# Optimization experiments

Measured on AMD Instinct MI355X. Metric: run time of the kernel, lower is better.

## Reference

```python
import jax, jax.numpy as jnp
import numpy as np

D_MODEL = 512
NUM_HEADS = 8
HEAD_DIM = D_MODEL // NUM_HEADS


def setup_inputs() -> dict:
    key = jax.random.key(0)
    k1, k2, k3, k4, k5 = jax.random.split(key, 5)
    B, S = 4, 2048
    hidden_states = jax.random.normal(k1, (B, S, D_MODEL), dtype=jnp.float32)
    attention_mask = jnp.ones((B, S), dtype=jnp.int32)
    scale = 1.0 / np.sqrt(D_MODEL)
    Wq = jax.random.normal(k2, (D_MODEL, D_MODEL), dtype=jnp.float32) * scale
    Wk = jax.random.normal(k3, (D_MODEL, D_MODEL), dtype=jnp.float32) * scale
    Wv = jax.random.normal(k4, (D_MODEL, D_MODEL), dtype=jnp.float32) * scale
    Wo = jax.random.normal(k5, (D_MODEL, D_MODEL), dtype=jnp.float32) * scale
    return {
        "hidden_states": hidden_states,
        "attention_mask": attention_mask,
        "Wq": Wq, "Wk": Wk, "Wv": Wv, "Wo": Wo,
        "window_size": 256,
    }


def reference(hidden_states, attention_mask, Wq, Wk, Wv, Wo, window_size):
    B, S, _ = hidden_states.shape
    H, Dh = NUM_HEADS, HEAD_DIM
    # torch Linear: y = x @ W.T  (weights are [out, in])
    q = (hidden_states @ Wq.T).reshape(B, S, H, Dh).transpose(0, 2, 1, 3)
    k = (hidden_states @ Wk.T).reshape(B, S, H, Dh).transpose(0, 2, 1, 3)
    v = (hidden_states @ Wv.T).reshape(B, S, H, Dh).transpose(0, 2, 1, 3)
    scores = jnp.einsum('bhnd,bhmd->bhnm', q, k) / jnp.sqrt(jnp.float32(Dh))
    # tril(diagonal=window_size-1): allow key m iff m - n <= window_size - 1
    n = jnp.arange(S)[:, None]
    m = jnp.arange(S)[None, :]
    band = (m - n) <= (window_size - 1)  # [S, S]
    allowed = band[None, None, :, :] & (attention_mask[:, None, None, :] != 0)
    scores = jnp.where(allowed, scores, -jnp.inf)
    attn = jax.nn.softmax(scores, axis=-1)
    out = jnp.einsum('bhnm,bhmd->bhnd', attn, v)
    out = out.transpose(0, 2, 1, 3).reshape(B, S, H * Dh)
    return out @ Wo.T
```

## Files before the change

kernel.cpp:

```cpp
#include <hip/hip_runtime.h>
#include <hip/hip_bf16.h>

#define BATCH 4
#define SEQ 2048
#define DM 512
#define NH 8
#define DH 64
#define WINDOW 256
#define NEGINF (-1e30f)
#define C_SCALE 0.18033688f
#define THR2 11.5415603f

typedef __attribute__((ext_vector_type(8)))  short bf16x8;
typedef __attribute__((ext_vector_type(4)))  float f32x4;
typedef __attribute__((ext_vector_type(16))) float f32x16;

__device__ __forceinline__ unsigned short f2bf(float f) {
    __hip_bfloat16 h = __float2bfloat16(f);
    union { __hip_bfloat16 h; unsigned short u; } cv; cv.h = h; return cv.u;
}
__device__ __forceinline__ unsigned int pack2(float a, float b) {
    return (unsigned int)f2bf(a) | ((unsigned int)f2bf(b) << 16);
}

__device__ __forceinline__ int swz128(int row, int byte_in_row) {
    return row * 128 + (byte_in_row ^ ((row & 7) << 4));
}

#define MFMA(a, b, c)   __builtin_amdgcn_mfma_f32_16x16x32_bf16(a, b, c, 0, 0, 0)
#define MFMA32(a, b, c) __builtin_amdgcn_mfma_f32_32x32x16_bf16(a, b, c, 0, 0, 0)

__global__ __launch_bounds__(256, 2) void gemm_qkv(
    const float* __restrict__ A,
    const float* __restrict__ W0f, const float* __restrict__ W1f,
    const float* __restrict__ W2f,
    unsigned short* __restrict__ C0, unsigned short* __restrict__ C1,
    unsigned short* __restrict__ C2, int M, int N, int K, int vtz)
{
    const float* W = (blockIdx.z == 0) ? W0f : (blockIdx.z == 1) ? W1f : W2f;
    unsigned short* C = (blockIdx.z == 0) ? C0 : (blockIdx.z == 1) ? C1 : C2;

    __shared__ unsigned short SMEM[2 * 2 * 128 * 64];

    const int tid  = threadIdx.x;
    const int m0   = blockIdx.x * 128;
    const int n0   = blockIdx.y * 128;
    const int lane = tid & 63;
    const int wv   = tid >> 6;
    const int wm   = wv >> 1, wn = wv & 1;
    const int g    = lane >> 4;
    const int lr   = lane & 15;
    const int r0   = tid >> 2;
    const int cgrp = tid & 3;
    const int NIT  = K / 64;

    f32x4 acc[4][4];
#pragma unroll
    for (int i = 0; i < 4; ++i)
#pragma unroll
        for (int j = 0; j < 4; ++j) { f32x4 z = {0.f,0.f,0.f,0.f}; acc[i][j] = z; }

    float4 pa[2][4], pwf[2][4];
    auto issue = [&](int it) {
        const int k0 = it * 64;
#pragma unroll
        for (int rr = 0; rr < 2; ++rr) {
            const float* sa = A + (size_t)(m0 + r0 + 64 * rr) * K + k0 + cgrp * 16;
            const float* sw = W + (size_t)(n0 + r0 + 64 * rr) * K + k0 + cgrp * 16;
#pragma unroll
            for (int c = 0; c < 4; ++c) {
                pa[rr][c]  = *reinterpret_cast<const float4*>(sa + 4 * c);
                pwf[rr][c] = *reinterpret_cast<const float4*>(sw + 4 * c);
            }
        }
    };
    auto writeLDS = [&](int buf) {
        unsigned short* As = SMEM + buf * 2 * 128 * 64;
        unsigned short* Ws = As + 128 * 64;
#pragma unroll
        for (int rr = 0; rr < 2; ++rr) {
            const int r = r0 + 64 * rr;
#pragma unroll
            for (int c = 0; c < 4; ++c) {
                const float4 va = pa[rr][c];
                uint2 wa; wa.x = pack2(va.x, va.y); wa.y = pack2(va.z, va.w);
                *reinterpret_cast<uint2*>((char*)As + swz128(r, cgrp * 32 + 8 * c)) = wa;
                const float4 vw = pwf[rr][c];
                uint2 ww; ww.x = pack2(vw.x, vw.y); ww.y = pack2(vw.z, vw.w);
                *reinterpret_cast<uint2*>((char*)Ws + swz128(r, cgrp * 32 + 8 * c)) = ww;
            }
        }
    };

    issue(0);
    writeLDS(0);
    issue(1);

    for (int it = 0; it < NIT; ++it) {
        const int cur = it & 1;
        __syncthreads();
        if (it + 1 < NIT) writeLDS(cur ^ 1);
        if (it + 2 < NIT) issue(it + 2);

        const unsigned short* As = SMEM + cur * 2 * 128 * 64;
        const unsigned short* Ws = As + 128 * 64;
#pragma unroll
        for (int ks = 0; ks < 2; ++ks) {
            bf16x8 af[4], bfr[4];
#pragma unroll
            for (int i = 0; i < 4; ++i)
                af[i] = *reinterpret_cast<const bf16x8*>(
                    (char*)As + swz128(64 * wm + 16 * i + lr, 64 * ks + 16 * g));
#pragma unroll
            for (int j = 0; j < 4; ++j)
                bfr[j] = *reinterpret_cast<const bf16x8*>(
                    (char*)Ws + swz128(64 * wn + 16 * j + lr, 64 * ks + 16 * g));
#pragma unroll
            for (int i = 0; i < 4; ++i)
#pragma unroll
                for (int j = 0; j < 4; ++j)
                    acc[i][j] = MFMA(af[i], bfr[j], acc[i][j]);
        }
    }

    if ((int)blockIdx.z == vtz) {
        __syncthreads();
        unsigned short* T = SMEM;
#pragma unroll
        for (int i = 0; i < 4; ++i)
#pragma unroll
            for (int j = 0; j < 4; ++j) {
                const int col  = 64 * wn + 16 * j + lr;
                const int rowb = 64 * wm + 16 * i + 4 * g;
                uint2 v;
                v.x = pack2(acc[i][j][0], acc[i][j][1]);
                v.y = pack2(acc[i][j][2], acc[i][j][3]);
                *reinterpret_cast<uint2*>(&T[col * 136 + rowb]) = v;
            }
        __syncthreads();
        const int col = tid >> 1, hf = tid & 1;
        const int bb  = m0 >> 11;
        unsigned short* dst = C + ((size_t)bb * DM + n0 + col) * SEQ
                                + (m0 & (SEQ - 1)) + 64 * hf;
        const unsigned short* src = &T[col * 136 + 64 * hf];
#pragma unroll
        for (int c = 0; c < 8; ++c)
            *reinterpret_cast<uint4*>(dst + 8 * c) =
                *reinterpret_cast<const uint4*>(src + 8 * c);
        return;
    }

#pragma unroll
    for (int i = 0; i < 4; ++i)
#pragma unroll
        for (int j = 0; j < 4; ++j) {
            const int col = n0 + 64 * wn + 16 * j + lr;
#pragma unroll
            for (int r = 0; r < 4; ++r) {
                const int row = m0 + 64 * wm + 16 * i + 4 * g + r;
                C[(size_t)row * N + col] = f2bf(acc[i][j][r]);
            }
        }
}

__global__ __launch_bounds__(256, 2) void gemm_out(
    const unsigned short* __restrict__ A,
    const float* __restrict__ Wf,
    float* __restrict__ C, int M, int N, int K)
{
    __shared__ unsigned short SMEM[2 * (128 * 64 + 64 * 64)];

    const int tid  = threadIdx.x;
    const int m0   = blockIdx.x * 128;
    const int n0   = blockIdx.y * 64;
    const int lane = tid & 63;
    const int wv   = tid >> 6;
    const int g    = lane >> 4;
    const int lr   = lane & 15;
    const int r0   = tid >> 2;
    const int cgrp = tid & 3;
    const int NIT  = K / 64;

    f32x4 acc[2][4];
#pragma unroll
    for (int i = 0; i < 2; ++i)
#pragma unroll
        for (int j = 0; j < 4; ++j) { f32x4 z = {0.f,0.f,0.f,0.f}; acc[i][j] = z; }

    uint4  pa[2][2];
    float4 pwf[4];
    auto issue = [&](int it) {
        const int k0 = it * 64;
#pragma unroll
        for (int rr = 0; rr < 2; ++rr) {
            const unsigned short* sa =
                A + (size_t)(m0 + r0 + 64 * rr) * K + k0 + cgrp * 16;
            pa[rr][0] = *reinterpret_cast<const uint4*>(sa);
            pa[rr][1] = *reinterpret_cast<const uint4*>(sa + 8);
        }
        const float* sw = Wf + (size_t)(n0 + r0) * K + k0 + cgrp * 16;
#pragma unroll
        for (int c = 0; c < 4; ++c)
            pwf[c] = *reinterpret_cast<const float4*>(sw + 4 * c);
    };
    auto writeLDS = [&](int buf) {
        unsigned short* As = SMEM + buf * (128 * 64 + 64 * 64);
        unsigned short* Ws = As + 128 * 64;
#pragma unroll
        for (int rr = 0; rr < 2; ++rr) {
            const int r = r0 + 64 * rr;
            *reinterpret_cast<uint4*>((char*)As + swz128(r, cgrp * 32))      = pa[rr][0];
            *reinterpret_cast<uint4*>((char*)As + swz128(r, cgrp * 32 + 16)) = pa[rr][1];
        }
#pragma unroll
        for (int c = 0; c < 4; ++c) {
            const float4 vw = pwf[c];
            uint2 ww; ww.x = pack2(vw.x, vw.y); ww.y = pack2(vw.z, vw.w);
            *reinterpret_cast<uint2*>((char*)Ws + swz128(r0, cgrp * 32 + 8 * c)) = ww;
        }
    };

    issue(0);
    writeLDS(0);
    issue(1);

    for (int it = 0; it < NIT; ++it) {
        const int cur = it & 1;
        __syncthreads();
        if (it + 1 < NIT) writeLDS(cur ^ 1);
        if (it + 2 < NIT) issue(it + 2);

        const unsigned short* As = SMEM + cur * (128 * 64 + 64 * 64);
        const unsigned short* Ws = As + 128 * 64;
#pragma unroll
        for (int ks = 0; ks < 2; ++ks) {
            bf16x8 af[2], bfr[4];
#pragma unroll
            for (int i = 0; i < 2; ++i)
                af[i] = *reinterpret_cast<const bf16x8*>(
                    (char*)As + swz128(32 * wv + 16 * i + lr, 64 * ks + 16 * g));
#pragma unroll
            for (int j = 0; j < 4; ++j)
                bfr[j] = *reinterpret_cast<const bf16x8*>(
                    (char*)Ws + swz128(16 * j + lr, 64 * ks + 16 * g));
#pragma unroll
            for (int i = 0; i < 2; ++i)
#pragma unroll
                for (int j = 0; j < 4; ++j)
                    acc[i][j] = MFMA(af[i], bfr[j], acc[i][j]);
        }
    }

#pragma unroll
    for (int i = 0; i < 2; ++i)
#pragma unroll
        for (int j = 0; j < 4; ++j) {
            const int col = n0 + 16 * j + lr;
#pragma unroll
            for (int r = 0; r < 4; ++r) {
                const int row = m0 + 32 * wv + 16 * i + 4 * g + r;
                C[(size_t)row * N + col] = acc[i][j][r];
            }
        }
}

__global__ __launch_bounds__(256) void attn_mfma32(
    const unsigned short* __restrict__ Q, const unsigned short* __restrict__ K,
    const unsigned short* __restrict__ VtG, const int* __restrict__ amask,
    unsigned short* __restrict__ AO)
{
    __shared__ unsigned short Ks[2][64 * 64];
    __shared__ unsigned short Vt[2][64 * 64];

    const int tid = threadIdx.x;
    const int x   = (int)blockIdx.x;
    const int r_  = (x < 256) ? x : 767 - x;
    const int qb  = 15 - (r_ >> 5);
    const int bh  = r_ & 31;
    const int n0  = qb * 128;
    const int b = bh >> 3, h = bh & 7;

    const int lane = tid & 63;
    const int wv   = tid >> 6;
    const int ql   = lane & 31;
    const int hb   = lane >> 5;

    const int qrow  = n0 + 32 * wv + ql;
    const int qminw = n0 + 32 * wv;
    const int qmaxw = qminw + 31;

    bf16x8 qf[4];
    {
        const unsigned short* qp =
            Q + (size_t)(b * SEQ + qrow) * DM + h * DH + 8 * hb;
#pragma unroll
        for (int st = 0; st < 4; ++st)
            qf[st] = *reinterpret_cast<const bf16x8*>(qp + 16 * st);
    }

    f32x16 o[2];
#pragma unroll
    for (int i = 0; i < 16; ++i) { o[0][i] = 0.f; o[1][i] = 0.f; }
    float m_run = NEGINF, l_run = 0.f;

    int ntiles = (n0 + 127 + WINDOW - 1) / 64 + 1;
    if (ntiles > SEQ / 64) ntiles = SEQ / 64;

    const int r_st = tid & 63;
    const int half = tid >> 6;
    const int vd   = tid >> 2;
    const int vc   = (tid & 3) * 8;
    const unsigned short* kpt = K + (size_t)(b * SEQ + r_st) * DM + h * DH + 16 * half;
    const unsigned short* vpt = VtG + ((size_t)b * DM + h * DH + vd) * SEQ + vc;
    const int* amp = amask + (size_t)b * SEQ + r_st;

    uint4 kr0, kr1, vv0, vv1; int mr = 1;
    auto issue = [&](int tt) {
        const unsigned short* kp = kpt + (size_t)tt * 64 * DM;
        kr0 = *reinterpret_cast<const uint4*>(kp);
        kr1 = *reinterpret_cast<const uint4*>(kp + 8);
        const unsigned short* vp = vpt + tt * 64;
        vv0 = *reinterpret_cast<const uint4*>(vp);
        vv1 = *reinterpret_cast<const uint4*>(vp + 32);
        mr = amp[tt * 64];
    };
    auto writeKV = [&](int buf) {
        *reinterpret_cast<uint4*>((char*)Ks[buf] + swz128(r_st, 32 * half))      = kr0;
        *reinterpret_cast<uint4*>((char*)Ks[buf] + swz128(r_st, 32 * half + 16)) = kr1;
        *reinterpret_cast<uint4*>((char*)Vt[buf] + swz128(vd, 2 * vc))           = vv0;
        *reinterpret_cast<uint4*>((char*)Vt[buf] + swz128(vd, 2 * vc + 64))      = vv1;
    };

    unsigned long long mw0 = ~0ULL, mw1 = ~0ULL;

    issue(0);
    writeKV(0);
    mw0 = __ballot(mr != 0);
    issue(1);

    for (int t = 0; t < ntiles; ++t) {
        const int cur = t & 1;
        const int kv0 = t * 64;
        __syncthreads();
        if (t + 1 < ntiles) {
            writeKV(cur ^ 1);
            const unsigned long long bw = __ballot(mr != 0);
            if (cur == 0) mw1 = bw; else mw0 = bw;
        }
        if (t + 2 < ntiles) issue(t + 2);

        if (kv0 > qmaxw + (WINDOW - 1)) continue;

        const unsigned long long mwt = cur ? mw1 : mw0;
        const bool fullband =
            ((kv0 + 63 - qminw) <= (WINDOW - 1)) && (mwt == ~0ULL);

        f32x16 s[2];
        __builtin_amdgcn_s_setprio(1);
#pragma unroll
        for (int T = 0; T < 2; ++T) {
            f32x16 z;
#pragma unroll
            for (int i = 0; i < 16; ++i) z[i] = 0.f;
#pragma unroll
            for (int st = 0; st < 4; ++st) {
                bf16x8 kf = *reinterpret_cast<const bf16x8*>(
                    (char*)Ks[cur] + swz128(32 * T + ql, 32 * st + 16 * hb));
                z = MFMA32(kf, qf[st], z);
            }
            s[T] = z;
        }
        __builtin_amdgcn_s_setprio(0);

        if (!fullband) {
            const int lim = qrow + (WINDOW - 1) - kv0;
#pragma unroll
            for (int T = 0; T < 2; ++T)
#pragma unroll
                for (int rg = 0; rg < 16; ++rg) {
                    const int kvi = 32 * T + (rg & 3) + 8 * (rg >> 2) + 4 * hb;
                    const bool ok = (kvi <= lim) && ((mwt >> kvi) & 1ULL);
                    s[T][rg] = ok ? s[T][rg] : NEGINF;
                }
        }

        float tmax = NEGINF;
#pragma unroll
        for (int T = 0; T < 2; ++T)
#pragma unroll
            for (int rg = 0; rg < 16; ++rg) tmax = fmaxf(tmax, s[T][rg]);
        tmax = fmaxf(tmax, __shfl_xor(tmax, 32));
        const float tm2 = tmax * C_SCALE;

        if (!__all(tm2 - m_run <= THR2)) {
            const float mn = fmaxf(m_run, tm2);
            const float sc = exp2f(m_run - mn);
            m_run = mn; l_run *= sc;
#pragma unroll
            for (int rg = 0; rg < 16; ++rg) { o[0][rg] *= sc; o[1][rg] *= sc; }
        }

        float ls = 0.f;
        unsigned int pw[16];
#pragma unroll
        for (int T = 0; T < 2; ++T)
#pragma unroll
            for (int i = 0; i < 8; ++i) {
                const float p0 = exp2f(fmaf(s[T][2 * i],     C_SCALE, -m_run));
                const float p1 = exp2f(fmaf(s[T][2 * i + 1], C_SCALE, -m_run));
                ls += p0 + p1;
                unsigned int r;
                asm("v_cvt_pk_bf16_f32 %0, %1, %2" : "=v"(r) : "v"(p0), "v"(p1));
                pw[8 * T + i] = r;
            }
        ls += __shfl_xor(ls, 32);
        l_run += ls;

        __builtin_amdgcn_s_setprio(1);
#pragma unroll
        for (int c = 0; c < 4; ++c) {
            const int base = 8 * (c >> 1) + 4 * (c & 1);
            unsigned int a0 = pw[base],     b0 = pw[base + 2];
            unsigned int a1 = pw[base + 1], b1 = pw[base + 3];
            asm("v_permlane32_swap_b32 %0, %1" : "+v"(a0), "+v"(b0));
            asm("v_permlane32_swap_b32 %0, %1" : "+v"(a1), "+v"(b1));
            union { unsigned int w[4]; bf16x8 v; } pf;
            pf.w[0] = a0; pf.w[1] = a1; pf.w[2] = b0; pf.w[3] = b1;
#pragma unroll
            for (int dt = 0; dt < 2; ++dt) {
                bf16x8 vf = *reinterpret_cast<const bf16x8*>(
                    (char*)Vt[cur] + swz128(32 * dt + ql, 32 * c + 16 * hb));
                o[dt] = MFMA32(vf, pf.v, o[dt]);
            }
        }
        __builtin_amdgcn_s_setprio(0);
    }

    const float inv = 1.f / l_run;
    unsigned short* op = AO + (size_t)(b * SEQ + qrow) * DM + h * DH;
#pragma unroll
    for (int dt = 0; dt < 2; ++dt)
#pragma unroll
        for (int p = 0; p < 4; ++p) {
            const float f0 = o[dt][4 * p]     * inv, f1 = o[dt][4 * p + 1] * inv;
            const float f2 = o[dt][4 * p + 2] * inv, f3 = o[dt][4 * p + 3] * inv;
            unsigned int w0, w1;
            asm("v_cvt_pk_bf16_f32 %0, %1, %2" : "=v"(w0) : "v"(f0), "v"(f1));
            asm("v_cvt_pk_bf16_f32 %0, %1, %2" : "=v"(w1) : "v"(f2), "v"(f3));
            uint2 st; st.x = w0; st.y = w1;
            *reinterpret_cast<uint2*>(op + 32 * dt + 8 * p + 4 * hb) = st;
        }
}

extern "C" void kernel_launch(void* const* d_in, const int* in_sizes, int n_in,
                              void* d_out, int out_size, void* d_ws, size_t ws_size,
                              hipStream_t stream) {
    const float* hs    = (const float*)d_in[0];
    const int*   amask = (const int*)  d_in[1];
    const float* Wq    = (const float*)d_in[2];
    const float* Wk    = (const float*)d_in[3];
    const float* Wv    = (const float*)d_in[4];
    const float* Wo    = (const float*)d_in[5];
    float* out = (float*)d_out;

    const size_t tok = (size_t)BATCH * SEQ * DM;
    unsigned short* Qb  = (unsigned short*)d_ws;
    unsigned short* Kb  = Qb + tok;
    unsigned short* VtG = Kb + tok;
    unsigned short* AOb = VtG + tok;

    const int M = BATCH * SEQ;

    dim3 gQKV(M / 128, DM / 128, 3);
    gemm_qkv<<<gQKV, 256, 0, stream>>>(hs, Wq, Wk, Wv, Qb, Kb, VtG, M, DM, DM, 2);

    attn_mfma32<<<dim3(512), 256, 0, stream>>>(Qb, Kb, VtG, amask, AOb);

    dim3 gOut(M / 128, DM / 64);
    gemm_out<<<gOut, 256, 0, stream>>>(AOb, Wo, out, M, DM, DM);
}
```

Measured before the change: 116.0 us.

## Stage 128-key KV tiles per barrier and use tree reductions in attention

The attention loop now loads and stages two 64-key sub-tiles (128 keys) per iteration with double buffering, which halves the number of block-wide barriers and global-load issue points. It also replaces the serial max and sum chains with pairwise tree reductions and adds a cheaper masking path when the padding mask tile is all ones. In exchange, LDS use doubles to 64KB per block and more prefetch registers are held, which may reduce occupancy. Coarser tiles can also load some keys beyond the window that the 64-key loop would not have touched.

```diff
diff --git a/kernel.cpp b/kernel.cpp
--- a/kernel.cpp
+++ b/kernel.cpp
@@ -269,8 +269,8 @@
     const unsigned short* __restrict__ VtG, const int* __restrict__ amask,
     unsigned short* __restrict__ AO)
 {
-    __shared__ unsigned short Ks[2][64 * 64];
-    __shared__ unsigned short Vt[2][64 * 64];
+    __shared__ unsigned short Ks[2][2][64 * 64];
+    __shared__ unsigned short Vt[2][2][64 * 64];
 
     const int tid = threadIdx.x;
     const int x   = (int)blockIdx.x;
@@ -303,8 +303,8 @@
     for (int i = 0; i < 16; ++i) { o[0][i] = 0.f; o[1][i] = 0.f; }
     float m_run = NEGINF, l_run = 0.f;
 
-    int ntiles = (n0 + 127 + WINDOW - 1) / 64 + 1;
-    if (ntiles > SEQ / 64) ntiles = SEQ / 64;
+    int nt = (n0 + 127 + WINDOW - 1) / 128 + 1;
+    if (nt > SEQ / 128) nt = SEQ / 128;
 
     const int r_st = tid & 63;
     const int half = tid >> 6;
@@ -314,126 +314,161 @@
     const unsigned short* vpt = VtG + ((size_t)b * DM + h * DH + vd) * SEQ + vc;
     const int* amp = amask + (size_t)b * SEQ + r_st;
 
-    uint4 kr0, kr1, vv0, vv1; int mr = 1;
+    uint4 kr[4], vv[4]; int mr0 = 1, mr1 = 1;
     auto issue = [&](int tt) {
-        const unsigned short* kp = kpt + (size_t)tt * 64 * DM;
-        kr0 = *reinterpret_cast<const uint4*>(kp);
-        kr1 = *reinterpret_cast<const uint4*>(kp + 8);
-        const unsigned short* vp = vpt + tt * 64;
-        vv0 = *reinterpret_cast<const uint4*>(vp);
-        vv1 = *reinterpret_cast<const uint4*>(vp + 32);
-        mr = amp[tt * 64];
+        const unsigned short* kp = kpt + (size_t)tt * 128 * DM;
+        kr[0] = *reinterpret_cast<const uint4*>(kp);
+        kr[1] = *reinterpret_cast<const uint4*>(kp + 8);
+        kr[2] = *reinterpret_cast<const uint4*>(kp + (size_t)64 * DM);
+        kr[3] = *reinterpret_cast<const uint4*>(kp + (size_t)64 * DM + 8);
+        const unsigned short* vp = vpt + tt * 128;
+        vv[0] = *reinterpret_cast<const uint4*>(vp);
+        vv[1] = *reinterpret_cast<const uint4*>(vp + 32);
+        vv[2] = *reinterpret_cast<const uint4*>(vp + 64);
+        vv[3] = *reinterpret_cast<const uint4*>(vp + 96);
+        mr0 = amp[tt * 128];
+        mr1 = amp[tt * 128 + 64];
     };
     auto writeKV = [&](int buf) {
-        *reinterpret_cast<uint4*>((char*)Ks[buf] + swz128(r_st, 32 * half))      = kr0;
-        *reinterpret_cast<uint4*>((char*)Ks[buf] + swz128(r_st, 32 * half + 16)) = kr1;
-        *reinterpret_cast<uint4*>((char*)Vt[buf] + swz128(vd, 2 * vc))           = vv0;
-        *reinterpret_cast<uint4*>((char*)Vt[buf] + swz128(vd, 2 * vc + 64))      = vv1;
+        *reinterpret_cast<uint4*>((char*)&Ks[buf][0][0] + swz128(r_st, 32 * half))      = kr[0];
+        *reinterpret_cast<uint4*>((char*)&Ks[buf][0][0] + swz128(r_st, 32 * half + 16)) = kr[1];
+        *reinterpret_cast<uint4*>((char*)&Ks[buf][1][0] + swz128(r_st, 32 * half))      = kr[2];
+        *reinterpret_cast<uint4*>((char*)&Ks[buf][1][0] + swz128(r_st, 32 * half + 16)) = kr[3];
+        *reinterpret_cast<uint4*>((char*)&Vt[buf][0][0] + swz128(vd, 2 * vc))           = vv[0];
+        *reinterpret_cast<uint4*>((char*)&Vt[buf][0][0] + swz128(vd, 2 * vc + 64))      = vv[1];
+        *reinterpret_cast<uint4*>((char*)&Vt[buf][1][0] + swz128(vd, 2 * vc))           = vv[2];
+        *reinterpret_cast<uint4*>((char*)&Vt[buf][1][0] + swz128(vd, 2 * vc + 64))      = vv[3];
     };
 
-    unsigned long long mw0 = ~0ULL, mw1 = ~0ULL;
+    unsigned long long mw00 = ~0ULL, mw01 = ~0ULL;
+    unsigned long long mw10 = ~0ULL, mw11 = ~0ULL;
 
     issue(0);
     writeKV(0);
-    mw0 = __ballot(mr != 0);
+    mw00 = __ballot(mr0 != 0); mw01 = __ballot(mr1 != 0);
     issue(1);
 
-    for (int t = 0; t < ntiles; ++t) {
+    for (int t = 0; t < nt; ++t) {
         const int cur = t & 1;
-        const int kv0 = t * 64;
         __syncthreads();
-        if (t + 1 < ntiles) {
+        if (t + 1 < nt) {
             writeKV(cur ^ 1);
-            const unsigned long long bw = __ballot(mr != 0);
-            if (cur == 0) mw1 = bw; else mw0 = bw;
-        }
-        if (t + 2 < ntiles) issue(t + 2);
-
-        if (kv0 > qmaxw + (WINDOW - 1)) continue;
-
-        const unsigned long long mwt = cur ? mw1 : mw0;
-        const bool fullband =
-            ((kv0 + 63 - qminw) <= (WINDOW - 1)) && (mwt == ~0ULL);
-
-        f32x16 s[2];
-        __builtin_amdgcn_s_setprio(1);
-#pragma unroll
-        for (int T = 0; T < 2; ++T) {
-            f32x16 z;
-#pragma unroll
-            for (int i = 0; i < 16; ++i) z[i] = 0.f;
-#pragma unroll
-            for (int st = 0; st < 4; ++st) {
-                bf16x8 kf = *reinterpret_cast<const bf16x8*>(
-                    (char*)Ks[cur] + swz128(32 * T + ql, 32 * st + 16 * hb));
-                z = MFMA32(kf, qf[st], z);
-            }
-            s[T] = z;
-        }
-        __builtin_amdgcn_s_setprio(0);
-
-        if (!fullband) {
-            const int lim = qrow + (WINDOW - 1) - kv0;
+            const unsigned long long b0 = __ballot(mr0 != 0);
+            const unsigned long long b1 = __ballot(mr1 != 0);
+            if (cur == 0) { mw10 = b0; mw11 = b1; } else { mw00 = b0; mw01 = b1; }
+        }
+        if (t + 2 < nt) issue(t + 2);
+
+        if (t * 128 > qmaxw + (WINDOW - 1)) continue;
+
+#pragma unroll
+        for (int sub = 0; sub < 2; ++sub) {
+            const int kv0 = t * 128 + 64 * sub;
+            if (kv0 > qmaxw + (WINDOW - 1)) continue;
+
+            const unsigned long long mwt =
+                (cur == 0) ? (sub ? mw01 : mw00) : (sub ? mw11 : mw10);
+            const bool allgood = (mwt == ~0ULL);
+            const bool fullband =
+                ((kv0 + 63 - qminw) <= (WINDOW - 1)) && allgood;
+            const unsigned short* KsB = &Ks[cur][sub][0];
+            const unsigned short* VtB = &Vt[cur][sub][0];
+
+            f32x16 s[2];
+            __builtin_amdgcn_s_setprio(1);
+#pragma unroll
+            for (int T = 0; T < 2; ++T) {
+                f32x16 z;
+#pragma unroll
+                for (int i = 0; i < 16; ++i) z[i] = 0.f;
+#pragma unroll
+                for (int st = 0; st < 4; ++st) {
+                    bf16x8 kf = *reinterpret_cast<const bf16x8*>(
+                        (char*)KsB + swz128(32 * T + ql, 32 * st + 16 * hb));
+                    z = MFMA32(kf, qf[st], z);
+                }
+                s[T] = z;
+            }
+            __builtin_amdgcn_s_setprio(0);
+
+            if (!fullband) {
+                const int lim = qrow + (WINDOW - 1) - kv0;
+                if (allgood) {
+#pragma unroll
+                    for (int T = 0; T < 2; ++T)
+#pragma unroll
+                        for (int rg = 0; rg < 16; ++rg) {
+                            const int kvi = 32 * T + (rg & 3) + 8 * (rg >> 2) + 4 * hb;
+                            s[T][rg] = (kvi <= lim) ? s[T][rg] : NEGINF;
+                        }
+                } else {
+#pragma unroll
+                    for (int T = 0; T < 2; ++T)
+#pragma unroll
+                        for (int rg = 0; rg < 16; ++rg) {
+                            const int kvi = 32 * T + (rg & 3) + 8 * (rg >> 2) + 4 * hb;
+                            const bool ok = (kvi <= lim) && ((mwt >> kvi) & 1ULL);
+                            s[T][rg] = ok ? s[T][rg] : NEGINF;
+                        }
+                }
+            }
+
+            float mx[16];
+#pragma unroll
+            for (int i = 0; i < 16; ++i) mx[i] = fmaxf(s[0][i], s[1][i]);
+#pragma unroll
+            for (int w = 8; w; w >>= 1)
+#pragma unroll
+                for (int i = 0; i < w; ++i) mx[i] = fmaxf(mx[i], mx[i + w]);
+            float tmax = fmaxf(mx[0], __shfl_xor(mx[0], 32));
+            const float tm2 = tmax * C_SCALE;
+
+            if (!__all(tm2 - m_run <= THR2)) {
+                const float mn = fmaxf(m_run, tm2);
+                const float sc = exp2f(m_run - mn);
+                m_run = mn; l_run *= sc;
+#pragma unroll
+                for (int rg = 0; rg < 16; ++rg) { o[0][rg] *= sc; o[1][rg] *= sc; }
+            }
+
+            float lp[16];
+            unsigned int pw[16];
 #pragma unroll
             for (int T = 0; T < 2; ++T)
 #pragma unroll
-                for (int rg = 0; rg < 16; ++rg) {
-                    const int kvi = 32 * T + (rg & 3) + 8 * (rg >> 2) + 4 * hb;
-                    const bool ok = (kvi <= lim) && ((mwt >> kvi) & 1ULL);
-                    s[T][rg] = ok ? s[T][rg] : NEGINF;
+                for (int i = 0; i < 8; ++i) {
+                    const float p0 = exp2f(fmaf(s[T][2 * i],     C_SCALE, -m_run));
+                    const float p1 = exp2f(fmaf(s[T][2 * i + 1], C_SCALE, -m_run));
+                    lp[8 * T + i] = p0 + p1;
+                    unsigned int r;
+                    asm("v_cvt_pk_bf16_f32 %0, %1, %2" : "=v"(r) : "v"(p0), "v"(p1));
+                    pw[8 * T + i] = r;
                 }
-        }
-
-        float tmax = NEGINF;
-#pragma unroll
-        for (int T = 0; T < 2; ++T)
-#pragma unroll
-            for (int rg = 0; rg < 16; ++rg) tmax = fmaxf(tmax, s[T][rg]);
-        tmax = fmaxf(tmax, __shfl_xor(tmax, 32));
-        const float tm2 = tmax * C_SCALE;
-
-        if (!__all(tm2 - m_run <= THR2)) {
-            const float mn = fmaxf(m_run, tm2);
-            const float sc = exp2f(m_run - mn);
-            m_run = mn; l_run *= sc;
-#pragma unroll
-            for (int rg = 0; rg < 16; ++rg) { o[0][rg] *= sc; o[1][rg] *= sc; }
-        }
-
-        float ls = 0.f;
-        unsigned int pw[16];
-#pragma unroll
-        for (int T = 0; T < 2; ++T)
-#pragma unroll
-            for (int i = 0; i < 8; ++i) {
-                const float p0 = exp2f(fmaf(s[T][2 * i],     C_SCALE, -m_run));
-                const float p1 = exp2f(fmaf(s[T][2 * i + 1], C_SCALE, -m_run));
-                ls += p0 + p1;
-                unsigned int r;
-                asm("v_cvt_pk_bf16_f32 %0, %1, %2" : "=v"(r) : "v"(p0), "v"(p1));
-                pw[8 * T + i] = r;
-            }
-        ls += __shfl_xor(ls, 32);
-        l_run += ls;
-
-        __builtin_amdgcn_s_setprio(1);
-#pragma unroll
-        for (int c = 0; c < 4; ++c) {
-            const int base = 8 * (c >> 1) + 4 * (c & 1);
-            unsigned int a0 = pw[base],     b0 = pw[base + 2];
-            unsigned int a1 = pw[base + 1], b1 = pw[base + 3];
-            asm("v_permlane32_swap_b32 %0, %1" : "+v"(a0), "+v"(b0));
-            asm("v_permlane32_swap_b32 %0, %1" : "+v"(a1), "+v"(b1));
-            union { unsigned int w[4]; bf16x8 v; } pf;
-            pf.w[0] = a0; pf.w[1] = a1; pf.w[2] = b0; pf.w[3] = b1;
-#pragma unroll
-            for (int dt = 0; dt < 2; ++dt) {
-                bf16x8 vf = *reinterpret_cast<const bf16x8*>(
-                    (char*)Vt[cur] + swz128(32 * dt + ql, 32 * c + 16 * hb));
-                o[dt] = MFMA32(vf, pf.v, o[dt]);
-            }
-        }
-        __builtin_amdgcn_s_setprio(0);
+#pragma unroll
+            for (int w = 8; w; w >>= 1)
+#pragma unroll
+                for (int i = 0; i < w; ++i) lp[i] += lp[i + w];
+            l_run += lp[0] + __shfl_xor(lp[0], 32);
+
+            __builtin_amdgcn_s_setprio(1);
+#pragma unroll
+            for (int c = 0; c < 4; ++c) {
+                const int base = 8 * (c >> 1) + 4 * (c & 1);
+                unsigned int a0 = pw[base],     b0 = pw[base + 2];
+                unsigned int a1 = pw[base + 1], b1 = pw[base + 3];
+                asm("v_permlane32_swap_b32 %0, %1" : "+v"(a0), "+v"(b0));
+                asm("v_permlane32_swap_b32 %0, %1" : "+v"(a1), "+v"(b1));
+                union { unsigned int w[4]; bf16x8 v; } pf;
+                pf.w[0] = a0; pf.w[1] = a1; pf.w[2] = b0; pf.w[3] = b1;
+#pragma unroll
+                for (int dt = 0; dt < 2; ++dt) {
+                    bf16x8 vf = *reinterpret_cast<const bf16x8*>(
+                        (char*)VtB + swz128(32 * dt + ql, 32 * c + 16 * hb));
+                    o[dt] = MFMA32(vf, pf.v, o[dt]);
+                }
+            }
+            __builtin_amdgcn_s_setprio(0);
+        }
     }
 
     const float inv = 1.f / l_run;
```

Measured after the change: 176.6 us. +52.2%, slower.

## Split attention KV tiles across wave pairs with 64-row query blocks and merge

Applied to the files above, without the earlier changes.

The attention kernel now handles 64 query rows per block instead of 128, and each pair of waves splits every 64-key tile into two 32-key halves, each keeping its own online-softmax state. At the end, the partial outputs are merged through shared memory using the running max and sum, which doubles the grid to 1024 blocks. The aim is more parallelism and shorter per-wave dependency chains on the banded attention. The cost is that each block does more K/V loading relative to its queries, plus an extra merge step and shared-memory traffic.

```diff
diff --git a/kernel.cpp b/kernel.cpp
--- a/kernel.cpp
+++ b/kernel.cpp
@@ -264,29 +264,30 @@
         }
 }
 
-__global__ __launch_bounds__(256) void attn_mfma32(
+__global__ __launch_bounds__(256) void attn_split64(
     const unsigned short* __restrict__ Q, const unsigned short* __restrict__ K,
     const unsigned short* __restrict__ VtG, const int* __restrict__ amask,
     unsigned short* __restrict__ AO)
 {
-    __shared__ unsigned short Ks[2][64 * 64];
-    __shared__ unsigned short Vt[2][64 * 64];
+    extern __shared__ unsigned short SMEM[];
 
     const int tid = threadIdx.x;
     const int x   = (int)blockIdx.x;
-    const int r_  = (x < 256) ? x : 767 - x;
-    const int qb  = 15 - (r_ >> 5);
+    const int r_  = (x < 512) ? x : 1535 - x;
+    const int qb  = 31 - (r_ >> 5);
     const int bh  = r_ & 31;
-    const int n0  = qb * 128;
+    const int n0  = qb * 64;
     const int b = bh >> 3, h = bh & 7;
 
     const int lane = tid & 63;
     const int wv   = tid >> 6;
+    const int qh   = wv >> 1;
+    const int kh   = wv & 1;
     const int ql   = lane & 31;
     const int hb   = lane >> 5;
 
-    const int qrow  = n0 + 32 * wv + ql;
-    const int qminw = n0 + 32 * wv;
+    const int qrow  = n0 + 32 * qh + ql;
+    const int qminw = n0 + 32 * qh;
     const int qmaxw = qminw + 31;
 
     bf16x8 qf[4];
@@ -303,7 +304,7 @@
     for (int i = 0; i < 16; ++i) { o[0][i] = 0.f; o[1][i] = 0.f; }
     float m_run = NEGINF, l_run = 0.f;
 
-    int ntiles = (n0 + 127 + WINDOW - 1) / 64 + 1;
+    int ntiles = (n0 + 63 + WINDOW - 1) / 64 + 1;
     if (ntiles > SEQ / 64) ntiles = SEQ / 64;
 
     const int r_st = tid & 63;
@@ -325,10 +326,12 @@
         mr = amp[tt * 64];
     };
     auto writeKV = [&](int buf) {
-        *reinterpret_cast<uint4*>((char*)Ks[buf] + swz128(r_st, 32 * half))      = kr0;
-        *reinterpret_cast<uint4*>((char*)Ks[buf] + swz128(r_st, 32 * half + 16)) = kr1;
-        *reinterpret_cast<uint4*>((char*)Vt[buf] + swz128(vd, 2 * vc))           = vv0;
-        *reinterpret_cast<uint4*>((char*)Vt[buf] + swz128(vd, 2 * vc + 64))      = vv1;
+        unsigned short* KsB = SMEM + buf * 4096;
+        unsigned short* VtB = SMEM + 8192 + buf * 4096;
+        *reinterpret_cast<uint4*>((char*)KsB + swz128(r_st, 32 * half))      = kr0;
+        *reinterpret_cast<uint4*>((char*)KsB + swz128(r_st, 32 * half + 16)) = kr1;
+        *reinterpret_cast<uint4*>((char*)VtB + swz128(vd, 2 * vc))           = vv0;
+        *reinterpret_cast<uint4*>((char*)VtB + swz128(vd, 2 * vc + 64))      = vv1;
     };
 
     unsigned long long mw0 = ~0ULL, mw1 = ~0ULL;
@@ -340,7 +343,6 @@
 
     for (int t = 0; t < ntiles; ++t) {
         const int cur = t & 1;
-        const int kv0 = t * 64;
         __syncthreads();
         if (t + 1 < ntiles) {
             writeKV(cur ^ 1);
@@ -349,46 +351,40 @@
         }
         if (t + 2 < ntiles) issue(t + 2);
 
-        if (kv0 > qmaxw + (WINDOW - 1)) continue;
+        const int kv0s = t * 64 + 32 * kh;
+        if (kv0s > qmaxw + (WINDOW - 1)) continue;
 
         const unsigned long long mwt = cur ? mw1 : mw0;
         const bool fullband =
-            ((kv0 + 63 - qminw) <= (WINDOW - 1)) && (mwt == ~0ULL);
-
-        f32x16 s[2];
+            ((kv0s + 31 - qminw) <= (WINDOW - 1)) && (mwt == ~0ULL);
+        const unsigned short* KsB = SMEM + cur * 4096;
+        const unsigned short* VtB = SMEM + 8192 + cur * 4096;
+
+        f32x16 s;
+#pragma unroll
+        for (int i = 0; i < 16; ++i) s[i] = 0.f;
         __builtin_amdgcn_s_setprio(1);
 #pragma unroll
-        for (int T = 0; T < 2; ++T) {
-            f32x16 z;
-#pragma unroll
-            for (int i = 0; i < 16; ++i) z[i] = 0.f;
-#pragma unroll
-            for (int st = 0; st < 4; ++st) {
-                bf16x8 kf = *reinterpret_cast<const bf16x8*>(
-                    (char*)Ks[cur] + swz128(32 * T + ql, 32 * st + 16 * hb));
-                z = MFMA32(kf, qf[st], z);
-            }
-            s[T] = z;
+        for (int st = 0; st < 4; ++st) {
+            bf16x8 kf = *reinterpret_cast<const bf16x8*>(
+                (char*)KsB + swz128(32 * kh + ql, 32 * st + 16 * hb));
+            s = MFMA32(kf, qf[st], s);
         }
         __builtin_amdgcn_s_setprio(0);
 
         if (!fullband) {
-            const int lim = qrow + (WINDOW - 1) - kv0;
-#pragma unroll
-            for (int T = 0; T < 2; ++T)
-#pragma unroll
-                for (int rg = 0; rg < 16; ++rg) {
-                    const int kvi = 32 * T + (rg & 3) + 8 * (rg >> 2) + 4 * hb;
-                    const bool ok = (kvi <= lim) && ((mwt >> kvi) & 1ULL);
-                    s[T][rg] = ok ? s[T][rg] : NEGINF;
-                }
+            const int lim = qrow + (WINDOW - 1) - t * 64;
+#pragma unroll
+            for (int rg = 0; rg < 16; ++rg) {
+                const int kvi = 32 * kh + (rg & 3) + 8 * (rg >> 2) + 4 * hb;
+                const bool ok = (kvi <= lim) && ((mwt >> kvi) & 1ULL);
+                s[rg] = ok ? s[rg] : NEGINF;
+            }
         }
 
         float tmax = NEGINF;
 #pragma unroll
-        for (int T = 0; T < 2; ++T)
-#pragma unroll
-            for (int rg = 0; rg < 16; ++rg) tmax = fmaxf(tmax, s[T][rg]);
+        for (int rg = 0; rg < 16; ++rg) tmax = fmaxf(tmax, s[rg]);
         tmax = fmaxf(tmax, __shfl_xor(tmax, 32));
         const float tm2 = tmax * C_SCALE;
 
@@ -401,27 +397,25 @@
         }
 
         float ls = 0.f;
-        unsigned int pw[16];
-#pragma unroll
-        for (int T = 0; T < 2; ++T)
-#pragma unroll
-            for (int i = 0; i < 8; ++i) {
-                const float p0 = exp2f(fmaf(s[T][2 * i],     C_SCALE, -m_run));
-                const float p1 = exp2f(fmaf(s[T][2 * i + 1], C_SCALE, -m_run));
-                ls += p0 + p1;
-                unsigned int r;
-                asm("v_cvt_pk_bf16_f32 %0, %1, %2" : "=v"(r) : "v"(p0), "v"(p1));
-                pw[8 * T + i] = r;
-            }
+        unsigned int pw8[8];
+#pragma unroll
+        for (int i = 0; i < 8; ++i) {
+            const float p0 = exp2f(fmaf(s[2 * i],     C_SCALE, -m_run));
+            const float p1 = exp2f(fmaf(s[2 * i + 1], C_SCALE, -m_run));
+            ls += p0 + p1;
+            unsigned int r;
+            asm("v_cvt_pk_bf16_f32 %0, %1, %2" : "=v"(r) : "v"(p0), "v"(p1));
+            pw8[i] = r;
+        }
         ls += __shfl_xor(ls, 32);
         l_run += ls;
 
         __builtin_amdgcn_s_setprio(1);
 #pragma unroll
-        for (int c = 0; c < 4; ++c) {
-            const int base = 8 * (c >> 1) + 4 * (c & 1);
-            unsigned int a0 = pw[base],     b0 = pw[base + 2];
-            unsigned int a1 = pw[base + 1], b1 = pw[base + 3];
+        for (int c = 0; c < 2; ++c) {
+            const int base = 4 * c;
+            unsigned int a0 = pw8[base],     b0 = pw8[base + 2];
+            unsigned int a1 = pw8[base + 1], b1 = pw8[base + 3];
             asm("v_permlane32_swap_b32 %0, %1" : "+v"(a0), "+v"(b0));
             asm("v_permlane32_swap_b32 %0, %1" : "+v"(a1), "+v"(b1));
             union { unsigned int w[4]; bf16x8 v; } pf;
@@ -429,27 +423,44 @@
 #pragma unroll
             for (int dt = 0; dt < 2; ++dt) {
                 bf16x8 vf = *reinterpret_cast<const bf16x8*>(
-                    (char*)Vt[cur] + swz128(32 * dt + ql, 32 * c + 16 * hb));
+                    (char*)VtB + swz128(32 * dt + ql, 64 * kh + 32 * c + 16 * hb));
                 o[dt] = MFMA32(vf, pf.v, o[dt]);
             }
         }
         __builtin_amdgcn_s_setprio(0);
     }
 
-    const float inv = 1.f / l_run;
-    unsigned short* op = AO + (size_t)(b * SEQ + qrow) * DM + h * DH;
-#pragma unroll
-    for (int dt = 0; dt < 2; ++dt)
-#pragma unroll
-        for (int p = 0; p < 4; ++p) {
-            const float f0 = o[dt][4 * p]     * inv, f1 = o[dt][4 * p + 1] * inv;
-            const float f2 = o[dt][4 * p + 2] * inv, f3 = o[dt][4 * p + 3] * inv;
-            unsigned int w0, w1;
-            asm("v_cvt_pk_bf16_f32 %0, %1, %2" : "=v"(w0) : "v"(f0), "v"(f1));
-            asm("v_cvt_pk_bf16_f32 %0, %1, %2" : "=v"(w1) : "v"(f2), "v"(f3));
-            uint2 st; st.x = w0; st.y = w1;
-            *reinterpret_cast<uint2*>(op + 32 * dt + 8 * p + 4 * hb) = st;
-        }
+    __syncthreads();
+    float* MRG = (float*)SMEM;
+    float* slot = MRG + ((size_t)qh * 64 + lane) * 34;
+    if (kh == 1) {
+#pragma unroll
+        for (int i = 0; i < 16; ++i) { slot[i] = o[0][i]; slot[16 + i] = o[1][i]; }
+        slot[32] = m_run; slot[33] = l_run;
+    }
+    __syncthreads();
+    if (kh == 0) {
+        const float m1 = slot[32], l1 = slot[33];
+        const float M  = fmaxf(m_run, m1);
+        const float w0 = exp2f(m_run - M);
+        const float w1 = exp2f(m1 - M);
+        const float inv = 1.f / (l_run * w0 + l1 * w1);
+        unsigned short* op = AO + (size_t)(b * SEQ + qrow) * DM + h * DH;
+#pragma unroll
+        for (int dt = 0; dt < 2; ++dt)
+#pragma unroll
+            for (int p = 0; p < 4; ++p) {
+                const float f0 = (o[dt][4 * p]     * w0 + slot[16 * dt + 4 * p]     * w1) * inv;
+                const float f1 = (o[dt][4 * p + 1] * w0 + slot[16 * dt + 4 * p + 1] * w1) * inv;
+                const float f2 = (o[dt][4 * p + 2] * w0 + slot[16 * dt + 4 * p + 2] * w1) * inv;
+                const float f3 = (o[dt][4 * p + 3] * w0 + slot[16 * dt + 4 * p + 3] * w1) * inv;
+                unsigned int w0p, w1p;
+                asm("v_cvt_pk_bf16_f32 %0, %1, %2" : "=v"(w0p) : "v"(f0), "v"(f1));
+                asm("v_cvt_pk_bf16_f32 %0, %1, %2" : "=v"(w1p) : "v"(f2), "v"(f3));
+                uint2 st; st.x = w0p; st.y = w1p;
+                *reinterpret_cast<uint2*>(op + 32 * dt + 8 * p + 4 * hb) = st;
+            }
+    }
 }
 
 extern "C" void kernel_launch(void* const* d_in, const int* in_sizes, int n_in,
@@ -474,7 +485,7 @@
     dim3 gQKV(M / 128, DM / 128, 3);
     gemm_qkv<<<gQKV, 256, 0, stream>>>(hs, Wq, Wk, Wv, Qb, Kb, VtG, M, DM, DM, 2);
 
-    attn_mfma32<<<dim3(512), 256, 0, stream>>>(Qb, Kb, VtG, amask, AOb);
+    attn_split64<<<dim3(1024), 256, 32768, stream>>>(Qb, Kb, VtG, amask, AOb);
 
     dim3 gOut(M / 128, DM / 64);
     gemm_out<<<gOut, 256, 0, stream>>>(AOb, Wo, out, M, DM, DM);
```

New measurement: 132.9 us. +14.5%, slower.
